# Optimization experiments

Hardware: AMD Instinct MI355X
Metric: run time of the kernel (lower is better)

Reference implementation:

```python
import jax, jax.numpy as jnp
import numpy as np

B, C, H, W = 4, 512, 128, 128
CQ = C // 8  # in_dim // reduction


def setup_inputs() -> dict:
    key = jax.random.key(0)
    ks = jax.random.split(key, 8)
    s = 1.0 / np.sqrt(C)
    return {
        "x": jax.random.normal(ks[0], (B, C, H, W), jnp.float32),
        "Wq": jax.random.normal(ks[1], (CQ, C), jnp.float32) * s,
        "bq": jax.random.normal(ks[2], (CQ,), jnp.float32) * 0.01,
        "Wk": jax.random.normal(ks[3], (CQ, C), jnp.float32) * s,
        "bk": jax.random.normal(ks[4], (CQ,), jnp.float32) * 0.01,
        "Wv": jax.random.normal(ks[5], (C, C), jnp.float32) * s,
        "bv": jax.random.normal(ks[6], (C,), jnp.float32) * 0.01,
        "gamma": jax.random.uniform(ks[7], (1,), jnp.float32) * 0.1,
    }


def reference(x, Wq, bq, Wk, bk, Wv, bv, gamma):
    b, c, h, w = x.shape
    cq = Wq.shape[0]
    # 1x1 convs == per-pixel GEMMs
    q = jnp.einsum('bchw,oc->bohw', x, Wq) + bq[None, :, None, None]
    k = jnp.einsum('bchw,oc->bohw', x, Wk) + bk[None, :, None, None]
    v = jnp.einsum('bchw,oc->bohw', x, Wv) + bv[None, :, None, None]

    # --- horizontal (row) attention ---
    qh = jnp.transpose(q, (0, 2, 3, 1)).reshape(b * h, w, cq)      # (BH, W, Cq)
    # faithful to torch .view(): raw reshape of (W,Cq) block -> (Cq,W), NOT a transpose
    kh = jnp.transpose(k, (0, 2, 3, 1)).reshape(b * h, cq, w)      # (BH, Cq, W)
    vh = jnp.transpose(v, (0, 2, 3, 1)).reshape(b * h, w, c)       # (BH, W, C)
    ah = jax.nn.softmax(jnp.matmul(qh, kh), axis=-1)               # (BH, W, W)
    ch = jnp.matmul(ah, vh).reshape(b, h, w, c).transpose(0, 3, 1, 2)

    # --- vertical (column) attention ---
    qv = jnp.transpose(q, (0, 3, 1, 2)).reshape(b * w, h, cq)      # faithful raw reshape of (Cq,H) -> (H,Cq)
    kv = jnp.transpose(k, (0, 3, 1, 2)).reshape(b * w, cq, h)      # (BW, Cq, H)
    vv = jnp.transpose(v, (0, 3, 1, 2)).reshape(b * w, h, c)       # faithful raw reshape
    av = jax.nn.softmax(jnp.matmul(qv, kv), axis=-1)               # (BW, H, H)
    cv = jnp.matmul(av, vv).reshape(b, w, h, c).transpose(0, 3, 2, 1)

    return gamma * (ch + cv) + x
```

## Files before the change

kernel.cpp:

```cpp
#include <hip/hip_runtime.h>
#include <stdint.h>

#define B_ 4
#define C_ 512
#define CQ_ 64
#define H_ 128
#define W_ 128
#define HW_ 16384

typedef unsigned short u16;
typedef unsigned int u32;
typedef __attribute__((ext_vector_type(8))) __bf16 bf16x8;
typedef __attribute__((ext_vector_type(4))) float f32x4;

__device__ __forceinline__ u16 f2bf(float f) {
    u32 v; __builtin_memcpy(&v, &f, 4);
    v = (v + 0x7FFFu + ((v >> 16) & 1u)) >> 16;
    return (u16)v;
}
__device__ __forceinline__ float bf2f(u16 a) {
    u32 v = ((u32)a) << 16; float f; __builtin_memcpy(&f, &v, 4); return f;
}

#define WS_XT  0u
#define WS_CV  0u
#define WS_Q   33554432u
#define WS_K   37748736u
#define WS_V   41943040u
#define WS_QT  75497472u
#define WS_KT  79691776u
#define WS_WB  75497472u
#define WS_VT  83886080u

__global__ __launch_bounds__(256) void prep_x(const float* __restrict__ x, u16* __restrict__ ws)
{
    __shared__ __align__(16) u16 tl[64][72];
    const int t = threadIdx.x;
    const int pt = blockIdx.x, ct = blockIdx.y, b = blockIdx.z;
    const int p0 = pt * 64, c0 = ct * 64;
    const float* xb = x + ((u32)(b*C_ + c0))*HW_ + p0;
    #pragma unroll
    for (int pass = 0; pass < 4; ++pass) {
        int ci = pass*256 + t, cl = ci >> 4, p4 = ci & 15;
        float4 d = *reinterpret_cast<const float4*>(xb + (u32)cl*HW_ + p4*4);
        tl[p4*4+0][cl] = f2bf(d.x); tl[p4*4+1][cl] = f2bf(d.y);
        tl[p4*4+2][cl] = f2bf(d.z); tl[p4*4+3][cl] = f2bf(d.w);
    }
    __syncthreads();
    u16* dst = ws + WS_XT + ((u32)((b<<14) + p0))*512 + c0;
    #pragma unroll
    for (int pass = 0; pass < 2; ++pass) {
        int ci = pass*256 + t, pr = ci >> 3, k8 = ci & 7;
        uint4 d = *reinterpret_cast<const uint4*>(&tl[pr][k8*8]);
        *reinterpret_cast<uint4*>(dst + (u32)pr*512 + k8*8) = d;
    }
}

__global__ __launch_bounds__(256) void prep_w(const float* __restrict__ Wq, const float* __restrict__ Wk,
                                              const float* __restrict__ Wv, u16* __restrict__ ws)
{
    const int f = (blockIdx.x*256 + threadIdx.x)*4;
    const float* src;
    if (f < 32768)      src = Wq + f;
    else if (f < 65536) src = Wk + (f - 32768);
    else                src = Wv + (f - 65536);
    float4 d = *reinterpret_cast<const float4*>(src);
    u16 e[4] = { f2bf(d.x), f2bf(d.y), f2bf(d.z), f2bf(d.w) };
    *reinterpret_cast<uint2*>(ws + WS_WB + f) = *reinterpret_cast<const uint2*>(e);
}

__global__ __launch_bounds__(256) void proj_kernel(const float* __restrict__ bq, const float* __restrict__ bk,
                                                   const float* __restrict__ bv, u16* __restrict__ ws)
{
    __shared__ __align__(16) u16 As[128][72];
    __shared__ __align__(16) u16 Bs[128][72];
    const int t = threadIdx.x;
    const int bm = blockIdx.x, bn = blockIdx.y, b = blockIdx.z;
    const int m0 = bm*128, p0 = bn*128;
    const u16* WB = ws + WS_WB;
    const u16* XT = ws + WS_XT + ((u32)((b<<14) + p0))*512;
    const int wv = t >> 6, ln = t & 63, quad = ln >> 4, col = ln & 15;
    const int mh = (wv>>1)*64, nh = (wv&1)*64;

    f32x4 acc[4][4];
    #pragma unroll
    for (int mt = 0; mt < 4; ++mt)
        #pragma unroll
        for (int nt = 0; nt < 4; ++nt) acc[mt][nt] = (f32x4){0.f,0.f,0.f,0.f};

    for (int c0 = 0; c0 < 512; c0 += 64) {
        #pragma unroll
        for (int pass = 0; pass < 4; ++pass) {
            int ci = pass*256 + t, row = ci >> 3, k8 = ci & 7;
            uint4 da = *reinterpret_cast<const uint4*>(WB + (u32)(m0+row)*512 + c0 + k8*8);
            *reinterpret_cast<uint4*>(&As[row][k8*8]) = da;
            uint4 db = *reinterpret_cast<const uint4*>(XT + (u32)row*512 + c0 + k8*8);
            *reinterpret_cast<uint4*>(&Bs[row][k8*8]) = db;
        }
        __syncthreads();
        #pragma unroll
        for (int ks = 0; ks < 2; ++ks) {
            const int kk = ks*32 + quad*8;
            bf16x8 am[4], bn_[4];
            #pragma unroll
            for (int mt = 0; mt < 4; ++mt) am[mt]  = *reinterpret_cast<const bf16x8*>(&As[mh + mt*16 + col][kk]);
            #pragma unroll
            for (int nt = 0; nt < 4; ++nt) bn_[nt] = *reinterpret_cast<const bf16x8*>(&Bs[nh + nt*16 + col][kk]);
            #pragma unroll
            for (int mt = 0; mt < 4; ++mt)
                #pragma unroll
                for (int nt = 0; nt < 4; ++nt)
                    acc[mt][nt] = __builtin_amdgcn_mfma_f32_16x16x32_bf16(am[mt], bn_[nt], acc[mt][nt], 0, 0, 0);
        }
        __syncthreads();
    }
    const int h = bn;
    #pragma unroll
    for (int mt = 0; mt < 4; ++mt) {
        const int obase = m0 + mh + mt*16 + quad*4;
        #pragma unroll
        for (int r = 0; r < 4; ++r) {
            const int o = obase + r;
            float bb; u16* dst;
            if (o < 64)       { bb = bq[o];     dst = ws + WS_Q + ((u32)((b<<6) + o))*HW_ + p0; }
            else if (o < 128) { bb = bk[o-64];  dst = ws + WS_K + ((u32)((b<<6) + (o-64)))*HW_ + p0; }
            else              { bb = bv[o-128]; dst = ws + WS_V + (u32)b*8388608u + (u32)h*65536u + (u32)(o-128)*128u; }
            #pragma unroll
            for (int nt = 0; nt < 4; ++nt) {
                int pl = nh + nt*16 + col;
                dst[pl] = f2bf(acc[mt][nt][r] + bb);
            }
        }
    }
}

__global__ __launch_bounds__(256) void transpose_qk(u16* __restrict__ ws)
{
    __shared__ u16 tl[64][70];
    const int t = threadIdx.x;
    const int tile = blockIdx.x, img = blockIdx.y;
    const int h0 = (tile >> 1) * 64, w0 = (tile & 1) * 64;
    const u16* src = ws + WS_Q + (u32)img * HW_;
    u16* dst = ws + WS_QT + (u32)img * HW_;
    #pragma unroll
    for (int pass = 0; pass < 2; ++pass) {
        int ci = pass*256 + t, hl = ci >> 3, w8 = ci & 7;
        uint4 d = *reinterpret_cast<const uint4*>(src + (u32)(h0+hl)*W_ + w0 + w8*8);
        const u16* e = reinterpret_cast<const u16*>(&d);
        #pragma unroll
        for (int j = 0; j < 8; ++j) tl[w8*8+j][hl] = e[j];
    }
    __syncthreads();
    #pragma unroll
    for (int pass = 0; pass < 4; ++pass) {
        int ci = pass*256 + t, wl = ci >> 4, h4 = ci & 15;
        uint2 d;
        d.x = *reinterpret_cast<const u32*>(&tl[wl][h4*4]);
        d.y = *reinterpret_cast<const u32*>(&tl[wl][h4*4+2]);
        *reinterpret_cast<uint2*>(dst + (u32)(w0+wl)*H_ + h0 + h4*4) = d;
    }
}

__global__ __launch_bounds__(256) void shuffle_v(u16* __restrict__ ws)
{
    __shared__ u16 tl[128][134];
    const int t = threadIdx.x;
    const int ct = blockIdx.x, h = blockIdx.y, b = blockIdx.z;
    const int c0 = ct * 128;
    const u16* src = ws + WS_V + (u32)b*8388608u + (u32)h*65536u + (u32)c0*128u;
    #pragma unroll
    for (int pass = 0; pass < 8; ++pass) {
        int ci = pass*256 + t, cl = ci >> 4, w8 = ci & 15;
        uint4 d = *reinterpret_cast<const uint4*>(src + (u32)cl*128u + w8*8);
        *reinterpret_cast<uint4*>(&tl[cl][w8*8]) = d;
    }
    __syncthreads();
    u16* dst = ws + WS_VT + (u32)b*8388608u;
    #pragma unroll
    for (int pass = 0; pass < 8; ++pass) {
        int ci = pass*256 + t;
        int w = ci >> 4, g = (ci >> 2) & 3, q4 = ci & 3;
        u16 e[8];
        #pragma unroll
        for (int jj = 0; jj < 8; ++jj)
            e[jj] = tl[4*(q4*8 + jj) + g][w];
        *reinterpret_cast<uint4*>(dst + (u32)w*65536u + (u32)(g*128 + h)*128u + (c0>>2) + q4*8)
            = *reinterpret_cast<const uint4*>(e);
    }
}

union __align__(16) ShAttn {
    struct QK { u16 q[128][72]; u16 kt[128][72]; } qk;
    u16 a[128][136];
};

__global__ __launch_bounds__(256) void hattn_kernel(const u16* __restrict__ ws, float* __restrict__ outp)
{
    __shared__ ShAttn sh;
    const int t = threadIdx.x;
    const int h = blockIdx.x, b = blockIdx.y;
    const u16* qsrc = ws + WS_Q + (u32)(b*CQ_)*HW_ + h*W_;
    const u16* ksrc = ws + WS_K + (u32)(b*CQ_)*HW_ + h*W_;

    for (int e = t; e < 8192; e += 256) {
        int cq = e >> 7, w = e & 127;
        sh.qk.q[w][cq] = qsrc[cq*HW_ + w];
        u16 kv = ksrc[cq*HW_ + w];
        sh.qk.kt[cq + ((w & 1) << 6)][w >> 1] = kv;
    }
    __syncthreads();

    const int wv = t >> 6, ln = t & 63, quad = ln >> 4, col = ln & 15;
    f32x4 accs[2][8];
    #pragma unroll
    for (int mt = 0; mt < 2; ++mt)
        #pragma unroll
        for (int nt = 0; nt < 8; ++nt) accs[mt][nt] = (f32x4){0.f,0.f,0.f,0.f};

    #pragma unroll
    for (int ks = 0; ks < 2; ++ks) {
        bf16x8 bfv[8];
        #pragma unroll
        for (int nt = 0; nt < 8; ++nt)
            bfv[nt] = *reinterpret_cast<const bf16x8*>(&sh.qk.kt[nt*16 + col][ks*32 + quad*8]);
        #pragma unroll
        for (int mt = 0; mt < 2; ++mt) {
            bf16x8 af = *reinterpret_cast<const bf16x8*>(&sh.qk.q[(wv*2 + mt)*16 + col][ks*32 + quad*8]);
            #pragma unroll
            for (int nt = 0; nt < 8; ++nt)
                accs[mt][nt] = __builtin_amdgcn_mfma_f32_16x16x32_bf16(af, bfv[nt], accs[mt][nt], 0, 0, 0);
        }
    }
    #pragma unroll
    for (int mt = 0; mt < 2; ++mt) {
        #pragma unroll
        for (int r = 0; r < 4; ++r) {
            float mx = accs[mt][0][r];
            #pragma unroll
            for (int nt = 1; nt < 8; ++nt) mx = fmaxf(mx, accs[mt][nt][r]);
            #pragma unroll
            for (int d = 1; d <= 8; d <<= 1) mx = fmaxf(mx, __shfl_xor(mx, d, 64));
            float sum = 0.f;
            #pragma unroll
            for (int nt = 0; nt < 8; ++nt) { float ev = __expf(accs[mt][nt][r] - mx); accs[mt][nt][r] = ev; sum += ev; }
            #pragma unroll
            for (int d = 1; d <= 8; d <<= 1) sum += __shfl_xor(sum, d, 64);
            float inv = 1.f / sum;
            #pragma unroll
            for (int nt = 0; nt < 8; ++nt) accs[mt][nt][r] *= inv;
        }
    }
    __syncthreads();
    #pragma unroll
    for (int mt = 0; mt < 2; ++mt)
        #pragma unroll
        for (int nt = 0; nt < 8; ++nt)
            #pragma unroll
            for (int r = 0; r < 4; ++r) {
                int w1 = (wv*2 + mt)*16 + quad*4 + r;
                int w2 = nt*16 + col;
                sh.a[w1][w2] = f2bf(accs[mt][nt][r]);
            }
    __syncthreads();

    const u16* vsrc = ws + WS_V + (u32)b*8388608u + (u32)h*65536u;
    float* chout = outp + (u32)(b*C_)*HW_ + h*W_;
    const int ccw = wv * 128;
    for (int mp = 0; mp < 4; ++mp) {
        f32x4 accv[2][8];
        #pragma unroll
        for (int mi = 0; mi < 2; ++mi)
            #pragma unroll
            for (int nt = 0; nt < 8; ++nt) accv[mi][nt] = (f32x4){0.f,0.f,0.f,0.f};
        #pragma unroll
        for (int ks = 0; ks < 4; ++ks) {
            bf16x8 bfv[8];
            #pragma unroll
            for (int nt = 0; nt < 8; ++nt)
                bfv[nt] = *reinterpret_cast<const bf16x8*>(&sh.a[nt*16 + col][ks*32 + quad*8]);
            #pragma unroll
            for (int mi = 0; mi < 2; ++mi) {
                int cct = ccw + (mp*2 + mi)*16;
                bf16x8 af = *reinterpret_cast<const bf16x8*>(&vsrc[(u32)(cct + col)*128u + ks*32 + quad*8]);
                #pragma unroll
                for (int nt = 0; nt < 8; ++nt)
                    accv[mi][nt] = __builtin_amdgcn_mfma_f32_16x16x32_bf16(af, bfv[nt], accv[mi][nt], 0, 0, 0);
            }
        }
        #pragma unroll
        for (int mi = 0; mi < 2; ++mi)
            #pragma unroll
            for (int nt = 0; nt < 8; ++nt)
                #pragma unroll
                for (int r = 0; r < 4; ++r) {
                    int cc = ccw + (mp*2 + mi)*16 + quad*4 + r;
                    int w1 = nt*16 + col;
                    chout[(u32)cc*HW_ + w1] = accv[mi][nt][r];
                }
    }
}

union __align__(16) ShV {
    struct QK { u16 q[128][72]; u16 kt[128][72]; } qk;
    u16 a[128][136];
};

__global__ __launch_bounds__(256) void vattn_kernel(u16* __restrict__ ws)
{
    __shared__ ShV sh;
    const int t = threadIdx.x;
    const int w = blockIdx.x, b = blockIdx.y;
    const u16* qTs = ws + WS_QT + (u32)(b*CQ_)*HW_ + w*H_;
    const u16* kTs = ws + WS_KT + (u32)(b*CQ_)*HW_ + w*H_;

    for (int e = t; e < 8192; e += 256) {
        int cq = e >> 7, hh = e & 127;
        sh.qk.q[2*cq + (hh >> 6)][hh & 63] = qTs[cq*HW_ + hh];
        sh.qk.kt[hh][cq] = kTs[cq*HW_ + hh];
    }
    __syncthreads();

    const int wv = t >> 6, ln = t & 63, quad = ln >> 4, col = ln & 15;
    f32x4 accs[2][8];
    #pragma unroll
    for (int mt = 0; mt < 2; ++mt)
        #pragma unroll
        for (int nt = 0; nt < 8; ++nt) accs[mt][nt] = (f32x4){0.f,0.f,0.f,0.f};

    #pragma unroll
    for (int ks = 0; ks < 2; ++ks) {
        bf16x8 bfv[8];
        #pragma unroll
        for (int nt = 0; nt < 8; ++nt)
            bfv[nt] = *reinterpret_cast<const bf16x8*>(&sh.qk.kt[nt*16 + col][ks*32 + quad*8]);
        #pragma unroll
        for (int mt = 0; mt < 2; ++mt) {
            bf16x8 af = *reinterpret_cast<const bf16x8*>(&sh.qk.q[(wv*2 + mt)*16 + col][ks*32 + quad*8]);
            #pragma unroll
            for (int nt = 0; nt < 8; ++nt)
                accs[mt][nt] = __builtin_amdgcn_mfma_f32_16x16x32_bf16(af, bfv[nt], accs[mt][nt], 0, 0, 0);
        }
    }
    #pragma unroll
    for (int mt = 0; mt < 2; ++mt) {
        #pragma unroll
        for (int r = 0; r < 4; ++r) {
            float mx = accs[mt][0][r];
            #pragma unroll
            for (int nt = 1; nt < 8; ++nt) mx = fmaxf(mx, accs[mt][nt][r]);
            #pragma unroll
            for (int d = 1; d <= 8; d <<= 1) mx = fmaxf(mx, __shfl_xor(mx, d, 64));
            float sum = 0.f;
            #pragma unroll
            for (int nt = 0; nt < 8; ++nt) { float ev = __expf(accs[mt][nt][r] - mx); accs[mt][nt][r] = ev; sum += ev; }
            #pragma unroll
            for (int d = 1; d <= 8; d <<= 1) sum += __shfl_xor(sum, d, 64);
            float inv = 1.f / sum;
            #pragma unroll
            for (int nt = 0; nt < 8; ++nt) accs[mt][nt][r] *= inv;
        }
    }
    __syncthreads();
    #pragma unroll
    for (int mt = 0; mt < 2; ++mt)
        #pragma unroll
        for (int nt = 0; nt < 8; ++nt)
            #pragma unroll
            for (int r = 0; r < 4; ++r) {
                int h1 = (wv*2 + mt)*16 + quad*4 + r;
                int h2 = nt*16 + col;
                sh.a[h1][h2] = f2bf(accs[mt][nt][r]);
            }
    __syncthreads();

    const u16* vvs = ws + WS_VT + ((u32)(b*W_ + w))*65536u;
    u16* cvout = ws + WS_CV + (u32)(b*C_)*HW_ + (u32)w*H_;
    for (int mp = 0; mp < 4; ++mp) {
        f32x4 accv[2][8];
        #pragma unroll
        for (int mi = 0; mi < 2; ++mi)
            #pragma unroll
            for (int nt = 0; nt < 8; ++nt) accv[mi][nt] = (f32x4){0.f,0.f,0.f,0.f};
        #pragma unroll
        for (int ks = 0; ks < 4; ++ks) {
            bf16x8 bfv[8];
            #pragma unroll
            for (int nt = 0; nt < 8; ++nt)
                bfv[nt] = *reinterpret_cast<const bf16x8*>(&sh.a[nt*16 + col][ks*32 + quad*8]);
            #pragma unroll
            for (int mi = 0; mi < 2; ++mi) {
                int ccrow = mp*128 + wv*32 + mi*16 + col;
                bf16x8 af = *reinterpret_cast<const bf16x8*>(&vvs[(u32)ccrow*128u + ks*32 + quad*8]);
                #pragma unroll
                for (int nt = 0; nt < 8; ++nt)
                    accv[mi][nt] = __builtin_amdgcn_mfma_f32_16x16x32_bf16(af, bfv[nt], accv[mi][nt], 0, 0, 0);
            }
        }
        #pragma unroll
        for (int mi = 0; mi < 2; ++mi)
            #pragma unroll
            for (int nt = 0; nt < 8; ++nt)
                #pragma unroll
                for (int r = 0; r < 4; ++r) {
                    int cc = mp*128 + wv*32 + mi*16 + quad*4 + r;
                    int h1 = nt*16 + col;
                    cvout[(u32)cc*HW_ + h1] = f2bf(accv[mi][nt][r]);
                }
    }
}

__global__ __launch_bounds__(256) void combine_kernel(const u16* __restrict__ ws, const float* __restrict__ x,
                                                      const float* __restrict__ gamma, float* __restrict__ outp)
{
    __shared__ u16 tl[64][70];
    const int t = threadIdx.x;
    const int tile = blockIdx.x, cc = blockIdx.y, b = blockIdx.z;
    const int h0 = (tile >> 1) * 64, w0 = (tile & 1) * 64;
    const float g = gamma[0];
    const u32 base = ((u32)(b*C_) + cc) * HW_;
    const u16* cvs = ws + WS_CV + base;
    #pragma unroll
    for (int pass = 0; pass < 2; ++pass) {
        int ci = pass*256 + t, wl = ci >> 3, h8 = ci & 7;
        uint4 d = *reinterpret_cast<const uint4*>(cvs + (u32)(w0+wl)*H_ + h0 + h8*8);
        const u16* e = reinterpret_cast<const u16*>(&d);
        #pragma unroll
        for (int j = 0; j < 8; ++j) tl[h8*8+j][wl] = e[j];
    }
    __syncthreads();
    #pragma unroll
    for (int pass = 0; pass < 4; ++pass) {
        int ci = pass*256 + t, hl = ci >> 4, w4 = ci & 15;
        u32 idx = base + (u32)(h0+hl)*W_ + w0 + w4*4;
        u32 p0 = *reinterpret_cast<const u32*>(&tl[hl][w4*4]);
        u32 p1 = *reinterpret_cast<const u32*>(&tl[hl][w4*4+2]);
        float4 ch = *reinterpret_cast<const float4*>(outp + idx);
        float4 xx = *reinterpret_cast<const float4*>(x + idx);
        float4 o;
        o.x = g*(ch.x + bf2f((u16)p0))         + xx.x;
        o.y = g*(ch.y + bf2f((u16)(p0 >> 16))) + xx.y;
        o.z = g*(ch.z + bf2f((u16)p1))         + xx.z;
        o.w = g*(ch.w + bf2f((u16)(p1 >> 16))) + xx.w;
        *reinterpret_cast<float4*>(outp + idx) = o;
    }
}

extern "C" void kernel_launch(void* const* d_in, const int* in_sizes, int n_in,
                              void* d_out, int out_size, void* d_ws, size_t ws_size,
                              hipStream_t stream)
{
    const float* x  = (const float*)d_in[0];
    const float* Wq = (const float*)d_in[1];
    const float* bq = (const float*)d_in[2];
    const float* Wk = (const float*)d_in[3];
    const float* bk = (const float*)d_in[4];
    const float* Wv = (const float*)d_in[5];
    const float* bv = (const float*)d_in[6];
    const float* gm = (const float*)d_in[7];
    float* out = (float*)d_out;
    u16* ws  = (u16*)d_ws;

    prep_x<<<dim3(256, 8, 4), 256, 0, stream>>>(x, ws);
    prep_w<<<dim3(320), 256, 0, stream>>>(Wq, Wk, Wv, ws);
    proj_kernel<<<dim3(5, 128, 4), 256, 0, stream>>>(bq, bk, bv, ws);
    transpose_qk<<<dim3(4, 512), 256, 0, stream>>>(ws);
    shuffle_v<<<dim3(4, 128, 4), 256, 0, stream>>>(ws);
    hattn_kernel<<<dim3(128, 4), 256, 0, stream>>>(ws, out);
    vattn_kernel<<<dim3(128, 4), 256, 0, stream>>>(ws);
    combine_kernel<<<dim3(4, 512, 4), 256, 0, stream>>>(ws, x, gm, out);
}
```

Measured before the change: 580.8 us.

## Prefetch next K-tile into registers and remap projection grid for XCD locality

The projection GEMM now loads the next 64-wide K slice from global memory into registers while MFMAs run on the current shared-memory tile, overlapping global latency with compute. The 3D grid is flattened to 1D and remapped so that consecutive groups of 8 blocks share the same weight tile across pixel tiles, which is intended to improve L2 reuse across the chiplets. This costs extra registers per thread and may lower occupancy. The projection is only one of several kernels, so any effect on total time is bounded by its share.

```diff
diff --git a/kernel.cpp b/kernel.cpp
--- a/kernel.cpp
+++ b/kernel.cpp
@@ -75,12 +75,17 @@
     __shared__ __align__(16) u16 As[128][72];
     __shared__ __align__(16) u16 Bs[128][72];
     const int t = threadIdx.x;
-    const int bm = blockIdx.x, bn = blockIdx.y, b = blockIdx.z;
+    const int bid = blockIdx.x;
+    const int x8 = bid & 7, q = bid >> 3;
+    const int pp = q / 5, bm = q - 5*pp;
+    const int p = pp*8 + x8;
+    const int b = p >> 7, bn = p & 127;
     const int m0 = bm*128, p0 = bn*128;
     const u16* WB = ws + WS_WB;
     const u16* XT = ws + WS_XT + ((u32)((b<<14) + p0))*512;
     const int wv = t >> 6, ln = t & 63, quad = ln >> 4, col = ln & 15;
     const int mh = (wv>>1)*64, nh = (wv&1)*64;
+    const int srow = t >> 3, sk8 = t & 7;
 
     f32x4 acc[4][4];
     #pragma unroll
@@ -88,16 +93,30 @@
         #pragma unroll
         for (int nt = 0; nt < 4; ++nt) acc[mt][nt] = (f32x4){0.f,0.f,0.f,0.f};
 
+    uint4 ra[4], rb[4];
+    #pragma unroll
+    for (int pass = 0; pass < 4; ++pass) {
+        int row = pass*32 + srow;
+        ra[pass] = *reinterpret_cast<const uint4*>(WB + (u32)(m0+row)*512 + sk8*8);
+        rb[pass] = *reinterpret_cast<const uint4*>(XT + (u32)row*512 + sk8*8);
+    }
+
     for (int c0 = 0; c0 < 512; c0 += 64) {
         #pragma unroll
         for (int pass = 0; pass < 4; ++pass) {
-            int ci = pass*256 + t, row = ci >> 3, k8 = ci & 7;
-            uint4 da = *reinterpret_cast<const uint4*>(WB + (u32)(m0+row)*512 + c0 + k8*8);
-            *reinterpret_cast<uint4*>(&As[row][k8*8]) = da;
-            uint4 db = *reinterpret_cast<const uint4*>(XT + (u32)row*512 + c0 + k8*8);
-            *reinterpret_cast<uint4*>(&Bs[row][k8*8]) = db;
+            int row = pass*32 + srow;
+            *reinterpret_cast<uint4*>(&As[row][sk8*8]) = ra[pass];
+            *reinterpret_cast<uint4*>(&Bs[row][sk8*8]) = rb[pass];
         }
         __syncthreads();
+        if (c0 + 64 < 512) {
+            #pragma unroll
+            for (int pass = 0; pass < 4; ++pass) {
+                int row = pass*32 + srow;
+                ra[pass] = *reinterpret_cast<const uint4*>(WB + (u32)(m0+row)*512 + c0 + 64 + sk8*8);
+                rb[pass] = *reinterpret_cast<const uint4*>(XT + (u32)row*512 + c0 + 64 + sk8*8);
+            }
+        }
         #pragma unroll
         for (int ks = 0; ks < 2; ++ks) {
             const int kk = ks*32 + quad*8;
@@ -462,7 +481,7 @@
 
     prep_x<<<dim3(256, 8, 4), 256, 0, stream>>>(x, ws);
     prep_w<<<dim3(320), 256, 0, stream>>>(Wq, Wk, Wv, ws);
-    proj_kernel<<<dim3(5, 128, 4), 256, 0, stream>>>(bq, bk, bv, ws);
+    proj_kernel<<<dim3(2560), 256, 0, stream>>>(bq, bk, bv, ws);
     transpose_qk<<<dim3(4, 512), 256, 0, stream>>>(ws);
     shuffle_v<<<dim3(4, 128, 4), 256, 0, stream>>>(ws);
     hattn_kernel<<<dim3(128, 4), 256, 0, stream>>>(ws, out);
```

After: 707.8 us. 1.22x slower.
